# Optimization experiments

Hardware: AMD Instinct MI355X
Metric: run time of the kernel (lower is better)

Reference implementation:

```python
import jax, jax.numpy as jnp
import numpy as np

R = 65536          # number of RoI proposals
D = 1024           # pooled feature dim (input_shape.channels)
C = 20             # num_classes (num_classes_stuff == 2 -> heads output num_classes)


def setup_inputs() -> dict:
    key = jax.random.key(0)
    k1, k2, k3 = jax.random.split(key, 3)
    x = jax.random.normal(k1, (R, D), dtype=jnp.float32)
    # xavier_uniform init for the two heads
    lim = float(np.sqrt(6.0 / (D + C)))
    W_cls = jax.random.uniform(k2, (C, D), dtype=jnp.float32, minval=-lim, maxval=lim)
    W_det = jax.random.uniform(k3, (C, D), dtype=jnp.float32, minval=-lim, maxval=lim)
    b_cls = jnp.zeros((C,), dtype=jnp.float32)
    b_det = jnp.zeros((C,), dtype=jnp.float32)
    return {"x": x, "W_cls": W_cls, "b_cls": b_cls, "W_det": W_det, "b_det": b_det}


def reference(x, W_cls, b_cls, W_det, b_det):
    # Flatten features if needed (torch.flatten(x, start_dim=1))
    x = x.reshape(x.shape[0], -1)
    cls_logits = x @ W_cls.T + b_cls          # [R, C]
    det_logits = x @ W_det.T + b_det          # [R, C]
    # WSDDN/JTSM MIL head: softmax over classes x softmax over proposals
    pred_cls = jax.nn.softmax(cls_logits, axis=1)
    pred_det = jax.nn.softmax(det_logits, axis=0)
    scores = pred_cls * pred_det              # [R, C] per-proposal per-class scores
    return scores
```

## Files before the change

kernel.cpp:

```cpp
#include <hip/hip_runtime.h>
#include <math.h>

#define NROWS 65536
#define NDIM  1024
#define NCLS  20
#define NOUT  40
#define KSEG  8
#define KLEN  128

__global__ __launch_bounds__(256) void repack_w_k(
    const float* __restrict__ Wc, const float* __restrict__ Wd,
    float* __restrict__ Wt, float* __restrict__ colsum)
{
    int i = blockIdx.x * 256 + threadIdx.x;
    int d = i / NOUT;
    int c = i % NOUT;
    float v = (c < NCLS) ? Wc[c * NDIM + d] : Wd[(c - NCLS) * NDIM + d];
    Wt[i] = v;
    if (i < NCLS) colsum[i] = 0.0f;
}

__global__ __launch_bounds__(512, 8) void main_gemm_k(
    const float* __restrict__ x,   const float* __restrict__ Wt,
    const float* __restrict__ bc,  const float* __restrict__ bd,
    float* __restrict__ out,       float* __restrict__ colsum)
{
    const int tid  = threadIdx.x;
    const int lane = tid & 63;
    const int w    = tid >> 6;
    const int wu   = __builtin_amdgcn_readfirstlane(w);
    const int row  = blockIdx.x * 64 + lane;

    const float* __restrict__ xr   = x  + (size_t)row * NDIM + wu * KLEN;
    const float* __restrict__ wseg = Wt + wu * KLEN * NOUT;

    float acc[NOUT];
#pragma unroll
    for (int c = 0; c < NOUT; ++c) acc[c] = 0.0f;

    for (int d0 = 0; d0 < KLEN; d0 += 8) {
        float4 c0 = ((const float4*)(xr + d0))[0];
        float4 c1 = ((const float4*)(xr + d0))[1];
        float cur[8];
        *(float4*)(cur + 0) = c0;
        *(float4*)(cur + 4) = c1;
        const float* __restrict__ wch = wseg + d0 * NOUT;
#pragma unroll
        for (int dd = 0; dd < 8; ++dd) {
            const float xs = cur[dd];
#pragma unroll
            for (int c = 0; c < NOUT; ++c)
                acc[c] = fmaf(xs, wch[dd * NOUT + c], acc[c]);
        }
    }

    __shared__ float red[NOUT][256];

    if (w >= 4) {
        const int s = tid - 256;
#pragma unroll
        for (int c = 0; c < NOUT; ++c) red[c][s] = acc[c];
    }
    __syncthreads();
    if (w < 4) {
#pragma unroll
        for (int c = 0; c < NOUT; ++c) acc[c] += red[c][tid];
    }
    __syncthreads();
    if (w == 2 || w == 3) {
        const int s = tid - 128;
#pragma unroll
        for (int c = 0; c < NOUT; ++c) red[c][s] = acc[c];
    }
    __syncthreads();
    if (w < 2) {
#pragma unroll
        for (int c = 0; c < NOUT; ++c) acc[c] += red[c][tid];
    }
    __syncthreads();
    if (w == 1) {
#pragma unroll
        for (int c = 0; c < NOUT; ++c) red[c][tid - 64] = acc[c];
    }
    __syncthreads();

    if (w == 0) {
#pragma unroll
        for (int c = 0; c < NOUT; ++c) acc[c] += red[c][lane];

#pragma unroll
        for (int c = 0; c < NCLS; ++c) acc[NCLS + c] = expf(acc[NCLS + c] + bd[c]);

#pragma unroll
        for (int c = 0; c < NCLS; ++c) {
            float v = acc[NCLS + c];
            v += __shfl_xor(v, 32, 64);
            v += __shfl_xor(v, 16, 64);
            v += __shfl_xor(v,  8, 64);
            v += __shfl_xor(v,  4, 64);
            v += __shfl_xor(v,  2, 64);
            v += __shfl_xor(v,  1, 64);
            if (lane == 0) atomicAdd(&colsum[c], v);
        }

        float m = -3.402823466e+38f;
#pragma unroll
        for (int c = 0; c < NCLS; ++c) { acc[c] += bc[c]; m = fmaxf(m, acc[c]); }
        float s = 0.0f;
#pragma unroll
        for (int c = 0; c < NCLS; ++c) { acc[c] = expf(acc[c] - m); s += acc[c]; }
        const float inv = 1.0f / s;

        float* __restrict__ orow = out + (size_t)row * NCLS;
#pragma unroll
        for (int i = 0; i < 5; ++i) {
            float4 v;
            v.x = acc[4*i + 0] * inv * acc[NCLS + 4*i + 0];
            v.y = acc[4*i + 1] * inv * acc[NCLS + 4*i + 1];
            v.z = acc[4*i + 2] * inv * acc[NCLS + 4*i + 2];
            v.w = acc[4*i + 3] * inv * acc[NCLS + 4*i + 3];
            ((float4*)orow)[i] = v;
        }
    }
}

__global__ void finalize_k(const float* __restrict__ colsum, float* __restrict__ inv)
{
    int c = threadIdx.x;
    if (c < NCLS) inv[c] = 1.0f / colsum[c];
}

__global__ __launch_bounds__(256) void scale_k(
    float* __restrict__ out, const float* __restrict__ inv)
{
    int i = blockIdx.x * 256 + threadIdx.x;
    int base = (i * 4) % NCLS;
    float4 v = ((float4*)out)[i];
    v.x *= inv[base + 0];
    v.y *= inv[base + 1];
    v.z *= inv[base + 2];
    v.w *= inv[base + 3];
    ((float4*)out)[i] = v;
}

extern "C" void kernel_launch(void* const* d_in, const int* in_sizes, int n_in,
                              void* d_out, int out_size, void* d_ws, size_t ws_size,
                              hipStream_t stream)
{
    const float* x  = (const float*)d_in[0];
    const float* Wc = (const float*)d_in[1];
    const float* bc = (const float*)d_in[2];
    const float* Wd = (const float*)d_in[3];
    const float* bd = (const float*)d_in[4];
    float* out = (float*)d_out;

    float* Wt     = (float*)d_ws;
    float* colsum = Wt + NDIM * NOUT;
    float* inv    = colsum + NCLS;

    repack_w_k<<<(NDIM * NOUT) / 256, 256, 0, stream>>>(Wc, Wd, Wt, colsum);
    main_gemm_k<<<NROWS / 64, 512, 0, stream>>>(x, Wt, bc, bd, out, colsum);
    finalize_k<<<1, 64, 0, stream>>>(colsum, inv);
    scale_k<<<(NROWS * NCLS / 4) / 256, 256, 0, stream>>>(out, inv);
}
```

Before: 598.7 us.

## Stage x tiles through padded LDS with coalesced loads, 4-wave K split

The GEMM kernel now loads each 64x128 tile of x with coalesced float4 reads across the block and stages it in padded shared memory. Each of 4 waves then reads its 32-wide K slice from LDS, instead of every lane doing strided per-row global reads over an 8-way K split. This targets uncoalesced global access to x. It adds two barriers per K tile and LDS traffic, cuts the block to 256 threads, and shortens the cross-wave reduction to two stages.

After: 620.3 us. 1.04x slower.

```diff
diff --git a/kernel.cpp b/kernel.cpp
--- a/kernel.cpp
+++ b/kernel.cpp
@@ -5,8 +5,9 @@
 #define NDIM  1024
 #define NCLS  20
 #define NOUT  40
-#define KSEG  8
-#define KLEN  128
+#define KT    128
+#define RPB   64
+#define PAD   129
 
 __global__ __launch_bounds__(256) void repack_w_k(
     const float* __restrict__ Wc, const float* __restrict__ Wd,
@@ -20,7 +21,7 @@
     if (i < NCLS) colsum[i] = 0.0f;
 }
 
-__global__ __launch_bounds__(512, 8) void main_gemm_k(
+__global__ __launch_bounds__(256) void main_gemm_k(
     const float* __restrict__ x,   const float* __restrict__ Wt,
     const float* __restrict__ bc,  const float* __restrict__ bd,
     float* __restrict__ out,       float* __restrict__ colsum)
@@ -29,78 +30,79 @@
     const int lane = tid & 63;
     const int w    = tid >> 6;
     const int wu   = __builtin_amdgcn_readfirstlane(w);
-    const int row  = blockIdx.x * 64 + lane;
+    const int row0 = blockIdx.x * RPB;
 
-    const float* __restrict__ xr   = x  + (size_t)row * NDIM + wu * KLEN;
-    const float* __restrict__ wseg = Wt + wu * KLEN * NOUT;
+    __shared__ float smem[RPB * PAD];
+
+    const int sr = tid >> 5;
+    const int sc = (tid & 31) * 4;
 
     float acc[NOUT];
 #pragma unroll
     for (int c = 0; c < NOUT; ++c) acc[c] = 0.0f;
 
-    for (int d0 = 0; d0 < KLEN; d0 += 8) {
-        float4 c0 = ((const float4*)(xr + d0))[0];
-        float4 c1 = ((const float4*)(xr + d0))[1];
-        float cur[8];
-        *(float4*)(cur + 0) = c0;
-        *(float4*)(cur + 4) = c1;
-        const float* __restrict__ wch = wseg + d0 * NOUT;
+    for (int t = 0; t < NDIM / KT; ++t) {
+        float4 v[8];
 #pragma unroll
-        for (int dd = 0; dd < 8; ++dd) {
-            const float xs = cur[dd];
+        for (int p = 0; p < 8; ++p) {
+            const int r = p * 8 + sr;
+            v[p] = *(const float4*)(x + (size_t)(row0 + r) * NDIM + t * KT + sc);
+        }
+#pragma unroll
+        for (int p = 0; p < 8; ++p) {
+            const int r = p * 8 + sr;
+            smem[r * PAD + sc + 0] = v[p].x;
+            smem[r * PAD + sc + 1] = v[p].y;
+            smem[r * PAD + sc + 2] = v[p].z;
+            smem[r * PAD + sc + 3] = v[p].w;
+        }
+        __syncthreads();
+
+        const float* __restrict__ wt = Wt + (size_t)(t * KT + wu * 32) * NOUT;
+#pragma unroll 4
+        for (int i = 0; i < 32; ++i) {
+            const float xs = smem[lane * PAD + wu * 32 + i];
 #pragma unroll
             for (int c = 0; c < NOUT; ++c)
-                acc[c] = fmaf(xs, wch[dd * NOUT + c], acc[c]);
+                acc[c] = fmaf(xs, wt[i * NOUT + c], acc[c]);
         }
+        __syncthreads();
     }
 
-    __shared__ float red[NOUT][256];
-
-    if (w >= 4) {
-        const int s = tid - 256;
-#pragma unroll
-        for (int c = 0; c < NOUT; ++c) red[c][s] = acc[c];
-    }
-    __syncthreads();
-    if (w < 4) {
-#pragma unroll
-        for (int c = 0; c < NOUT; ++c) acc[c] += red[c][tid];
-    }
-    __syncthreads();
-    if (w == 2 || w == 3) {
+    if (w >= 2) {
         const int s = tid - 128;
 #pragma unroll
-        for (int c = 0; c < NOUT; ++c) red[c][s] = acc[c];
+        for (int c = 0; c < NOUT; ++c) smem[c * 128 + s] = acc[c];
     }
     __syncthreads();
     if (w < 2) {
 #pragma unroll
-        for (int c = 0; c < NOUT; ++c) acc[c] += red[c][tid];
+        for (int c = 0; c < NOUT; ++c) acc[c] += smem[c * 128 + tid];
     }
     __syncthreads();
     if (w == 1) {
 #pragma unroll
-        for (int c = 0; c < NOUT; ++c) red[c][tid - 64] = acc[c];
+        for (int c = 0; c < NOUT; ++c) smem[c * 128 + (tid - 64)] = acc[c];
     }
     __syncthreads();
 
     if (w == 0) {
 #pragma unroll
-        for (int c = 0; c < NOUT; ++c) acc[c] += red[c][lane];
+        for (int c = 0; c < NOUT; ++c) acc[c] += smem[c * 128 + lane];
 
 #pragma unroll
         for (int c = 0; c < NCLS; ++c) acc[NCLS + c] = expf(acc[NCLS + c] + bd[c]);
 
 #pragma unroll
         for (int c = 0; c < NCLS; ++c) {
-            float v = acc[NCLS + c];
-            v += __shfl_xor(v, 32, 64);
-            v += __shfl_xor(v, 16, 64);
-            v += __shfl_xor(v,  8, 64);
-            v += __shfl_xor(v,  4, 64);
-            v += __shfl_xor(v,  2, 64);
-            v += __shfl_xor(v,  1, 64);
-            if (lane == 0) atomicAdd(&colsum[c], v);
+            float v2 = acc[NCLS + c];
+            v2 += __shfl_xor(v2, 32, 64);
+            v2 += __shfl_xor(v2, 16, 64);
+            v2 += __shfl_xor(v2,  8, 64);
+            v2 += __shfl_xor(v2,  4, 64);
+            v2 += __shfl_xor(v2,  2, 64);
+            v2 += __shfl_xor(v2,  1, 64);
+            if (lane == 0) atomicAdd(&colsum[c], v2);
         }
 
         float m = -3.402823466e+38f;
@@ -111,15 +113,15 @@
         for (int c = 0; c < NCLS; ++c) { acc[c] = expf(acc[c] - m); s += acc[c]; }
         const float inv = 1.0f / s;
 
-        float* __restrict__ orow = out + (size_t)row * NCLS;
+        float* __restrict__ orow = out + (size_t)(row0 + lane) * NCLS;
 #pragma unroll
         for (int i = 0; i < 5; ++i) {
-            float4 v;
-            v.x = acc[4*i + 0] * inv * acc[NCLS + 4*i + 0];
-            v.y = acc[4*i + 1] * inv * acc[NCLS + 4*i + 1];
-            v.z = acc[4*i + 2] * inv * acc[NCLS + 4*i + 2];
-            v.w = acc[4*i + 3] * inv * acc[NCLS + 4*i + 3];
-            ((float4*)orow)[i] = v;
+            float4 o;
+            o.x = acc[4*i + 0] * inv * acc[NCLS + 4*i + 0];
+            o.y = acc[4*i + 1] * inv * acc[NCLS + 4*i + 1];
+            o.z = acc[4*i + 2] * inv * acc[NCLS + 4*i + 2];
+            o.w = acc[4*i + 3] * inv * acc[NCLS + 4*i + 3];
+            ((float4*)orow)[i] = o;
         }
     }
 }
@@ -159,7 +161,7 @@
     float* inv    = colsum + NCLS;
 
     repack_w_k<<<(NDIM * NOUT) / 256, 256, 0, stream>>>(Wc, Wd, Wt, colsum);
-    main_gemm_k<<<NROWS / 64, 512, 0, stream>>>(x, Wt, bc, bd, out, colsum);
+    main_gemm_k<<<NROWS / RPB, 256, 0, stream>>>(x, Wt, bc, bd, out, colsum);
     finalize_k<<<1, 64, 0, stream>>>(colsum, inv);
     scale_k<<<(NROWS * NCLS / 4) / 256, 256, 0, stream>>>(out, inv);
 }
```
